# Optimization experiments

Hardware: AMD Instinct MI355X
Metric: run time of the kernel (lower is better)

The kernel has to match this reference:

```python
import jax, jax.numpy as jnp
import numpy as np
import math

N_FFT = 1024
HOP = 256
WIN = 1024
SR = 16000
N_MELS = 80
N_STFT = N_FFT // 2 + 1  # 513
B = 16
T_AUDIO = 320000


def _hz_to_mel_slaney(f):
    f = np.asarray(f, dtype=np.float64)
    mels = 3.0 * f / 200.0
    min_log_hz = 1000.0
    min_log_mel = 15.0
    logstep = math.log(6.4) / 27.0
    return np.where(f >= min_log_hz, min_log_mel + np.log(np.maximum(f, 1e-10) / min_log_hz) / logstep, mels)


def _mel_to_hz_slaney(m):
    m = np.asarray(m, dtype=np.float64)
    freqs = 200.0 * m / 3.0
    min_log_hz = 1000.0
    min_log_mel = 15.0
    logstep = math.log(6.4) / 27.0
    return np.where(m >= min_log_mel, min_log_hz * np.exp(logstep * (m - min_log_mel)), freqs)


def _melscale_fbanks(n_freqs, f_min, f_max, n_mels, sample_rate):
    # torchaudio.functional.melscale_fbanks with norm='slaney', mel_scale='slaney'
    all_freqs = np.linspace(0.0, sample_rate / 2.0, n_freqs)
    m_pts = np.linspace(_hz_to_mel_slaney(f_min), _hz_to_mel_slaney(f_max), n_mels + 2)
    f_pts = _mel_to_hz_slaney(m_pts)
    f_diff = f_pts[1:] - f_pts[:-1]                       # (n_mels+1,)
    slopes = f_pts[None, :] - all_freqs[:, None]          # (n_freqs, n_mels+2)
    down = -slopes[:, :-2] / f_diff[:-1]
    up = slopes[:, 2:] / f_diff[1:]
    fb = np.maximum(0.0, np.minimum(down, up))
    enorm = 2.0 / (f_pts[2:n_mels + 2] - f_pts[:n_mels])  # slaney norm
    fb = fb * enorm[None, :]
    return fb.astype(np.float32)                          # (n_freqs, n_mels)


def setup_inputs() -> dict:
    key = jax.random.key(0)
    wav = jax.random.normal(key, (B, 1, T_AUDIO), dtype=jnp.float32)
    # hann window, periodic
    n = np.arange(WIN, dtype=np.float64)
    window = (0.5 - 0.5 * np.cos(2.0 * np.pi * n / WIN)).astype(np.float32)
    mel_fbanks = _melscale_fbanks(N_STFT, 0.0, SR / 2.0, N_MELS, SR)
    k = np.arange(N_STFT, dtype=np.float64)[:, None]
    nn = np.arange(N_FFT, dtype=np.float64)[None, :]
    angle = -2.0 * np.pi * k * nn / N_FFT
    rfft_real_t = np.cos(angle).T.astype(np.float32)      # (n_fft, n_stft)
    rfft_imag_t = np.sin(angle).T.astype(np.float32)
    return {
        "wav_with_channel": wav,
        "window": jnp.asarray(window),
        "mel_fbanks": jnp.asarray(mel_fbanks),
        "rfft_real_t": jnp.asarray(rfft_real_t),
        "rfft_imag_t": jnp.asarray(rfft_imag_t),
    }


def reference(wav_with_channel, window, mel_fbanks, rfft_real_t, rfft_imag_t):
    wav = wav_with_channel[:, 0, :]                       # (B, T)
    pad = N_FFT // 2
    padded = jnp.pad(wav, ((0, 0), (pad, pad)), mode="reflect")
    padded_len = padded.shape[1]
    num_frames = (padded_len - WIN) // HOP + 1
    idx = jnp.arange(num_frames)[:, None] * HOP + jnp.arange(WIN)[None, :]
    frames = padded[:, idx]
    windowed = frames * window
    real = jnp.matmul(windowed, rfft_real_t)              # (B, F, n_stft)
    imag = jnp.matmul(windowed, rfft_imag_t)
    magnitude = jnp.sqrt(real * real + imag * imag)       # power == 1.0
    mel = jnp.matmul(magnitude, mel_fbanks)               # (B, F, n_mels)
    return jnp.transpose(mel, (0, 2, 1))                  # (B, n_mels, F)
```

## Files before the change

kernel.cpp:

```cpp
#include <hip/hip_runtime.h>
#include <cstddef>

#define HOP 256
#define NSTFT 513
#define N_MELS 80
#define T_AUDIO 320000
#define NUM_FRAMES 1251
#define NBATCH 16
#define TOTAL_FRAMES (NBATCH * NUM_FRAMES)

#define LOGSTEP 0.06875177742094913f
#define MEL_MAX 45.24564047f
#define DF 15.625f

__device__ __forceinline__ int reflect_idx(int j) {
    j = (j < 0) ? -j : j;
    j = (j >= T_AUDIO) ? (2 * T_AUDIO - 2 - j) : j;
    return j;
}

__device__ __forceinline__ int m1_of(int k) {
    const float f = k * DF;
    const float mel = (f < 1000.f) ? (3.0f / 200.0f) * f
                                   : 15.0f + logf(f * 1e-3f) * (1.0f / LOGSTEP);
    return (int)floorf(mel * (81.0f / MEL_MAX));
}

__device__ __forceinline__ int swz(int k) {
    return (k & ~15) | ((k ^ (k >> 4)) & 15);
}

#define DPP_XOR1 0xB1
#define DPP_XOR2 0x4E
#define DPP_XOR8 0x128
template<int CTRL>
__device__ __forceinline__ float dppf(float x) {
    return __int_as_float(__builtin_amdgcn_update_dpp(
        0, __float_as_int(x), CTRL, 0xF, 0xF, true));
}

template<class F>
__device__ __forceinline__ void cstage(float (&zr)[2][16], float (&zi)[2][16],
                                       float sg, float twr_, float twi_, F comm) {
    #pragma unroll
    for (int p = 0; p < 2; ++p) {
        #pragma unroll
        for (int r = 0; r < 16; ++r) {
            const float pr  = comm(zr[p][r]);
            const float pim = comm(zi[p][r]);
            const float qr = fmaf(sg, zr[p][r], pr);
            const float qi = fmaf(sg, zi[p][r], pim);
            zr[p][r] = fmaf(qr, twr_, -(qi * twi_));
            zi[p][r] = fmaf(qr, twi_, qi * twr_);
        }
    }
}

__global__ __launch_bounds__(256) void melspec_sfft6_kernel(
    const float* __restrict__ wav,
    const float* __restrict__ window,
    const float* __restrict__ fb,
    const float* __restrict__ cosT,
    const float* __restrict__ sinT,
    float* __restrict__ out)
{
    __shared__ float2 smag[4][512];
    __shared__ float2 wtab[512];
    __shared__ unsigned short ks[84];

    const int tid = threadIdx.x;
    const int lane = tid & 63;
    const int w = tid >> 6;
    const int g0 = (blockIdx.x * 4 + w) * 4;

    const int BREV4[16] = {0,8,4,12,2,10,6,14,1,9,5,13,3,11,7,15};
    const int SIG[16]   = {0,1,3,2,7,6,5,4,15,14,13,12,11,10,9,8};
    const float W16R[8] = {1.0f, 0.92387953251128674f, 0.70710678118654752f, 0.38268343236508977f,
                           0.0f, -0.38268343236508977f, -0.70710678118654752f, -0.92387953251128674f};
    const float W16I[8] = {0.0f, -0.38268343236508977f, -0.70710678118654752f, -0.92387953251128674f,
                           -1.0f, -0.92387953251128674f, -0.70710678118654752f, -0.38268343236508977f};

    for (int k = tid + 1; k <= 512; k += 256) {
        const int mc = m1_of(k);
        const int mp = m1_of(k - 1);
        if (k <= 511) {
            const float wu = (mc <= 79) ? fb[k * N_MELS + mc] : 0.0f;
            const float wd = (mc >= 1 && mc <= 80) ? fb[k * N_MELS + mc - 1] : 0.0f;
            wtab[swz(k)] = make_float2(wu, wd);
        }
        for (int m = mp + 1; m <= mc; ++m) ks[m] = (unsigned short)k;
        if (k == 1) ks[0] = 1;
    }
    __syncthreads();

    unsigned bf0, ff0, bf3;
    {
        const unsigned g = (unsigned)g0;
        bf0 = g / NUM_FRAMES; ff0 = g - bf0 * NUM_FRAMES;
        bf3 = (unsigned)(g0 + 3) / NUM_FRAMES;
    }

    float win[16];
    #pragma unroll
    for (int r = 0; r < 16; ++r) win[r] = window[r * 64 + lane];

    float zr[2][16], zi[2][16];
    if (bf0 == bf3) {
        const float* wb = wav + (size_t)bf0 * T_AUDIO;
        const int base = (int)ff0 * HOP - 512;
        float ch[28];
        #pragma unroll
        for (int c = 0; c < 28; ++c)
            ch[c] = wb[reflect_idx(base + c * 64 + lane)];
        #pragma unroll
        for (int r = 0; r < 16; ++r) {
            zr[0][r] = ch[r]      * win[r];
            zi[0][r] = ch[r + 4]  * win[r];
            zr[1][r] = ch[r + 8]  * win[r];
            zi[1][r] = ch[r + 12] * win[r];
        }
    } else {
        #pragma unroll
        for (int fi = 0; fi < 4; ++fi) {
            const unsigned g = (unsigned)(g0 + fi);
            const unsigned bb = g / NUM_FRAMES;
            const unsigned ffr = g - bb * NUM_FRAMES;
            const float* wb = wav + (size_t)bb * T_AUDIO;
            const int base = (int)ffr * HOP - 512;
            #pragma unroll
            for (int r = 0; r < 16; ++r) {
                const float v = wb[reflect_idx(base + r * 64 + lane)] * win[r];
                if (fi == 0) zr[0][r] = v;
                else if (fi == 1) zi[0][r] = v;
                else if (fi == 2) zr[1][r] = v;
                else zi[1][r] = v;
            }
        }
    }

    const float* twc = cosT + NSTFT;
    const float* tws = sinT + NSTFT;

    const float w1r = twc[lane];
    const float w1i = tws[lane];
    float wkr[16], wki[16];
    wkr[0] = 1.0f; wki[0] = 0.0f;
    #pragma unroll
    for (int k = 1; k < 16; ++k) {
        wkr[k] = wkr[k-1] * w1r - wki[k-1] * w1i;
        wki[k] = wkr[k-1] * w1i + wki[k-1] * w1r;
    }

    float c64[6], s64[6];
    #pragma unroll
    for (int t = 0; t < 6; ++t) {
        const int half = 32 >> t;
        const bool hi = (lane & half) != 0;
        const int jj = (lane & (half - 1)) << (t + 4);
        c64[t] = hi ? twc[jj] : 1.0f;
        s64[t] = hi ? tws[jj] : 0.0f;
    }

    #define CBFLY(ar, ai, br, bi, wr, wi) { \
        const float _tr = (ar) - (br), _ti = (ai) - (bi); \
        (ar) += (br); (ai) += (bi); \
        (br) = _tr * (wr) - _ti * (wi); \
        (bi) = _tr * (wi) + _ti * (wr); }

    #pragma unroll
    for (int p = 0; p < 2; ++p) {
        #pragma unroll
        for (int q = 0; q < 8; ++q) CBFLY(zr[p][q], zi[p][q], zr[p][q+8], zi[p][q+8], W16R[q], W16I[q]);
        #pragma unroll
        for (int g = 0; g < 16; g += 8)
            #pragma unroll
            for (int q = 0; q < 4; ++q) CBFLY(zr[p][g+q], zi[p][g+q], zr[p][g+q+4], zi[p][g+q+4], W16R[2*q], W16I[2*q]);
        #pragma unroll
        for (int g = 0; g < 16; g += 4)
            #pragma unroll
            for (int q = 0; q < 2; ++q) CBFLY(zr[p][g+q], zi[p][g+q], zr[p][g+q+2], zi[p][g+q+2], W16R[4*q], W16I[4*q]);
        #pragma unroll
        for (int g = 0; g < 16; g += 2) CBFLY(zr[p][g], zi[p][g], zr[p][g+1], zi[p][g+1], 1.0f, 0.0f);
    }

    #pragma unroll
    for (int r = 1; r < 16; ++r) {
        const float c1 = wkr[BREV4[r]];
        const float s1 = wki[BREV4[r]];
        #pragma unroll
        for (int p = 0; p < 2; ++p) {
            const float xr = zr[p][r], xi = zi[p][r];
            zr[p][r] = xr * c1 - xi * s1;
            zi[p][r] = xr * s1 + xi * c1;
        }
    }

    {
        float sg;
        sg = (lane & 32) ? -1.0f : 1.0f;
        cstage(zr, zi, sg, c64[0], s64[0], [](float v) { return __shfl_xor(v, 32); });
        sg = (lane & 16) ? -1.0f : 1.0f;
        cstage(zr, zi, sg, c64[1], s64[1], [](float v) { return __shfl_xor(v, 16); });
        sg = (lane & 8) ? -1.0f : 1.0f;
        cstage(zr, zi, sg, c64[2], s64[2], [](float v) { return dppf<DPP_XOR8>(v); });
        sg = (lane & 4) ? -1.0f : 1.0f;
        cstage(zr, zi, sg, c64[3], s64[3], [](float v) { return __shfl_xor(v, 4); });
        sg = (lane & 2) ? -1.0f : 1.0f;
        cstage(zr, zi, sg, c64[4], s64[4], [](float v) { return dppf<DPP_XOR2>(v); });
        sg = (lane & 1) ? -1.0f : 1.0f;
        cstage(zr, zi, sg, c64[5], s64[5], [](float v) { return dppf<DPP_XOR1>(v); });
    }

    const int k2 = (int)(__brev((unsigned)lane) >> 26);
    const int lp0 = (int)(__brev((unsigned)((64 - k2) & 63)) >> 26);
    #pragma unroll
    for (int p = 0; p < 2; ++p) {
        #pragma unroll
        for (int r = 0; r < 16; ++r) {
            float cx, cy;
            if (r == 0) { cx = __shfl(zr[p][0], lp0); cy = __shfl(zi[p][0], lp0); }
            else        { cx = __shfl_xor(zr[p][SIG[r]], 63); cy = __shfl_xor(zi[p][SIG[r]], 63); }
            const int k1 = BREV4[r];
            const int k = k2 * 16 + k1;
            if (k <= 511) {
                const float a = zr[p][r], b = zi[p][r];
                const float magA = 0.5f * sqrtf((a + cx) * (a + cx) + (b - cy) * (b - cy));
                const float magB = 0.5f * sqrtf((b + cy) * (b + cy) + (a - cx) * (a - cx));
                smag[w][(k & ~15) | (k1 ^ (k2 & 15))] = make_float2(magA, magB);
            }
        }
        #pragma unroll
        for (int i = 0; i < 3; ++i) {
            const int t2 = lane + 64 * i;
            if (t2 < 2 * N_MELS) {
                const int m = 79 - (t2 >> 1);
                const int fi = t2 & 1;
                const int ka = ks[m], kb = ks[m + 1], kc = ks[m + 2];
                float acc = 0.0f;
                for (int k = ka; k < kc; ++k) {
                    const int sl = swz(k);
                    const float2 mg = smag[w][sl];
                    const float2 wt = wtab[sl];
                    acc = fmaf(fi ? mg.y : mg.x, (k < kb) ? wt.x : wt.y, acc);
                }
                const unsigned g = (unsigned)(g0 + 2 * p + fi);
                const unsigned bb = g / NUM_FRAMES;
                const unsigned ff = g - bb * NUM_FRAMES;
                out[((size_t)bb * N_MELS + m) * NUM_FRAMES + ff] = acc;
            }
        }
    }
}

extern "C" void kernel_launch(void* const* d_in, const int* in_sizes, int n_in,
                              void* d_out, int out_size, void* d_ws, size_t ws_size,
                              hipStream_t stream) {
    const float* wav    = (const float*)d_in[0];
    const float* window = (const float*)d_in[1];
    const float* fb     = (const float*)d_in[2];
    const float* cosT   = (const float*)d_in[3];
    const float* sinT   = (const float*)d_in[4];
    float* out = (float*)d_out;

    const int blocks = TOTAL_FRAMES / 16;
    melspec_sfft6_kernel<<<blocks, 256, 0, stream>>>(wav, window, fb, cosT, sinT, out);
}
```

Baseline: 53.58 us.

## Compute mel filterbank via per-wave prefix sums instead of per-mel loops

Replaces the per-mel serial loop over FFT bins, which had variable trip counts and caused divergence, with a prefix-sum formulation. Each lane computes local weighted partial sums over its 16 bins. A wave-level scan across bin groups then produces cumulative sums written to shared memory, and each mel is obtained from three prefix lookups. The change also adds a fast unreflected path for interior frame loads and an occupancy hint in the launch bounds. It trades the divergent loops for extra shuffles and LDS traffic, and the prefix differencing may cost some float precision.

```diff
diff --git a/kernel.cpp b/kernel.cpp
--- a/kernel.cpp
+++ b/kernel.cpp
@@ -30,6 +30,10 @@
     return (k & ~15) | ((k ^ (k >> 4)) & 15);
 }
 
+__device__ __forceinline__ float bperm(int addr, float v) {
+    return __int_as_float(__builtin_amdgcn_ds_bpermute(addr, __float_as_int(v)));
+}
+
 #define DPP_XOR1 0xB1
 #define DPP_XOR2 0x4E
 #define DPP_XOR8 0x128
@@ -56,7 +60,7 @@
     }
 }
 
-__global__ __launch_bounds__(256) void melspec_sfft6_kernel(
+__global__ __launch_bounds__(256, 5) void melspec_ps_kernel(
     const float* __restrict__ wav,
     const float* __restrict__ window,
     const float* __restrict__ fb,
@@ -64,7 +68,7 @@
     const float* __restrict__ sinT,
     float* __restrict__ out)
 {
-    __shared__ float2 smag[4][512];
+    __shared__ float2 psb[4][512];
     __shared__ float2 wtab[512];
     __shared__ unsigned short ks[84];
 
@@ -80,16 +84,19 @@
     const float W16I[8] = {0.0f, -0.38268343236508977f, -0.70710678118654752f, -0.92387953251128674f,
                            -1.0f, -0.92387953251128674f, -0.70710678118654752f, -0.38268343236508977f};
 
-    for (int k = tid + 1; k <= 512; k += 256) {
+    if (tid == 0) { ks[81] = 512; ks[82] = 512; }
+    for (int k = tid; k <= 512; k += 256) {
         const int mc = m1_of(k);
-        const int mp = m1_of(k - 1);
         if (k <= 511) {
-            const float wu = (mc <= 79) ? fb[k * N_MELS + mc] : 0.0f;
-            const float wd = (mc >= 1 && mc <= 80) ? fb[k * N_MELS + mc - 1] : 0.0f;
+            const float wu = (mc >= 0 && mc <= 79) ? 0.5f * fb[k * N_MELS + mc] : 0.0f;
+            const float wd = (mc >= 1 && mc <= 80) ? 0.5f * fb[k * N_MELS + mc - 1] : 0.0f;
             wtab[swz(k)] = make_float2(wu, wd);
         }
-        for (int m = mp + 1; m <= mc; ++m) ks[m] = (unsigned short)k;
-        if (k == 1) ks[0] = 1;
+        if (k >= 1) {
+            const int mp = m1_of(k - 1);
+            for (int m = mp + 1; m <= mc; ++m) ks[m] = (unsigned short)k;
+            if (k == 1) ks[0] = 1;
+        }
     }
     __syncthreads();
 
@@ -109,9 +116,15 @@
         const float* wb = wav + (size_t)bf0 * T_AUDIO;
         const int base = (int)ff0 * HOP - 512;
         float ch[28];
-        #pragma unroll
-        for (int c = 0; c < 28; ++c)
-            ch[c] = wb[reflect_idx(base + c * 64 + lane)];
+        if (base >= 0 && base + 27 * 64 + 63 < T_AUDIO) {
+            #pragma unroll
+            for (int c = 0; c < 28; ++c)
+                ch[c] = wb[base + c * 64 + lane];
+        } else {
+            #pragma unroll
+            for (int c = 0; c < 28; ++c)
+                ch[c] = wb[reflect_idx(base + c * 64 + lane)];
+        }
         #pragma unroll
         for (int r = 0; r < 16; ++r) {
             zr[0][r] = ch[r]      * win[r];
@@ -211,44 +224,72 @@
         cstage(zr, zi, sg, c64[5], s64[5], [](float v) { return dppf<DPP_XOR1>(v); });
     }
 
-    const int k2 = (int)(__brev((unsigned)lane) >> 26);
-    const int lp0 = (int)(__brev((unsigned)((64 - k2) & 63)) >> 26);
+    const int k2c = (int)(__brev((unsigned)lane) >> 26);
+    const int lp0 = (int)(__brev((unsigned)((64 - k2c) & 63)) >> 26);
+    const int k2m16 = (k2c & 31) * 16;
+    const int k2c4 = k2c << 2;
+
     #pragma unroll
     for (int p = 0; p < 2; ++p) {
+        float mgA[16], mgB[16];
         #pragma unroll
         for (int r = 0; r < 16; ++r) {
             float cx, cy;
             if (r == 0) { cx = __shfl(zr[p][0], lp0); cy = __shfl(zi[p][0], lp0); }
             else        { cx = __shfl_xor(zr[p][SIG[r]], 63); cy = __shfl_xor(zi[p][SIG[r]], 63); }
-            const int k1 = BREV4[r];
-            const int k = k2 * 16 + k1;
-            if (k <= 511) {
-                const float a = zr[p][r], b = zi[p][r];
-                const float magA = 0.5f * sqrtf((a + cx) * (a + cx) + (b - cy) * (b - cy));
-                const float magB = 0.5f * sqrtf((b + cy) * (b + cy) + (a - cx) * (a - cx));
-                smag[w][(k & ~15) | (k1 ^ (k2 & 15))] = make_float2(magA, magB);
-            }
-        }
-        #pragma unroll
-        for (int i = 0; i < 3; ++i) {
-            const int t2 = lane + 64 * i;
-            if (t2 < 2 * N_MELS) {
-                const int m = 79 - (t2 >> 1);
-                const int fi = t2 & 1;
-                const int ka = ks[m], kb = ks[m + 1], kc = ks[m + 2];
-                float acc = 0.0f;
-                for (int k = ka; k < kc; ++k) {
-                    const int sl = swz(k);
-                    const float2 mg = smag[w][sl];
-                    const float2 wt = wtab[sl];
-                    acc = fmaf(fi ? mg.y : mg.x, (k < kb) ? wt.x : wt.y, acc);
+            const float a = zr[p][r], b = zi[p][r];
+            mgA[r] = sqrtf((a + cx) * (a + cx) + (b - cy) * (b - cy));
+            mgB[r] = sqrtf((b + cy) * (b + cy) + (a - cx) * (a - cx));
+        }
+
+        auto mel_pass = [&](const float (&mg)[16], int fi) {
+            float ru = 0.f, rd = 0.f;
+            #pragma unroll
+            for (int k1 = 0; k1 < 16; ++k1) {
+                const int r = BREV4[k1];
+                const float2 wt = wtab[swz(k2m16 + k1)];
+                ru = fmaf(mg[r], wt.x, ru);
+                rd = fmaf(mg[r], wt.y, rd);
+            }
+            float vu = bperm(k2c4, ru), vd = bperm(k2c4, rd);
+            const float tu = vu, td = vd;
+            #pragma unroll
+            for (int s = 1; s <= 16; s <<= 1) {
+                const float au = __shfl_up(vu, s);
+                const float ad = __shfl_up(vd, s);
+                if (lane >= s) { vu += au; vd += ad; }
+            }
+            const float eu = bperm(k2c4, vu - tu);
+            const float ed = bperm(k2c4, vd - td);
+            if (!(lane & 1)) {
+                float pu = eu, pd = ed;
+                #pragma unroll
+                for (int k1 = 0; k1 < 16; ++k1) {
+                    const int r = BREV4[k1];
+                    const float2 wt = wtab[swz(k2m16 + k1)];
+                    pu = fmaf(mg[r], wt.x, pu);
+                    pd = fmaf(mg[r], wt.y, pd);
+                    psb[w][swz(k2m16 + k1)] = make_float2(pu, pd);
                 }
-                const unsigned g = (unsigned)(g0 + 2 * p + fi);
-                const unsigned bb = g / NUM_FRAMES;
-                const unsigned ff = g - bb * NUM_FRAMES;
-                out[((size_t)bb * N_MELS + m) * NUM_FRAMES + ff] = acc;
-            }
-        }
+            }
+            #pragma unroll
+            for (int ii = 0; ii < 2; ++ii) {
+                const int m = lane + 64 * ii;
+                if (m < N_MELS) {
+                    const int ka = ks[m], kb = ks[m + 1], kc = ks[m + 2];
+                    const float2 Pa = psb[w][swz(ka - 1)];
+                    const float2 Pb = psb[w][swz(kb - 1)];
+                    const float2 Pc = psb[w][swz(kc - 1)];
+                    const float mel = (Pb.x - Pa.x) + (Pc.y - Pb.y);
+                    const unsigned g = (unsigned)(g0 + 2 * p + fi);
+                    const unsigned bb = g / NUM_FRAMES;
+                    const unsigned ff = g - bb * NUM_FRAMES;
+                    out[((size_t)bb * N_MELS + m) * NUM_FRAMES + ff] = mel;
+                }
+            }
+        };
+        mel_pass(mgA, 0);
+        mel_pass(mgB, 1);
     }
 }
 
@@ -263,5 +304,5 @@
     float* out = (float*)d_out;
 
     const int blocks = TOTAL_FRAMES / 16;
-    melspec_sfft6_kernel<<<blocks, 256, 0, stream>>>(wav, window, fb, cosT, sinT, out);
-}
+    melspec_ps_kernel<<<blocks, 256, 0, stream>>>(wav, window, fb, cosT, sinT, out);
+}
```

After: 133.9 us. 150% more time.

## Premultiply mel weights into LDS products, use permlane swaps and fast-path loads

Applied to the files above, without the earlier changes.

The magnitude stage now multiplies each bin's magnitude by its two filterbank weights (with the 0.5 scale folded into the table) and stores the products in two per-wave LDS arrays. The mel reduction then only sums selected products using two accumulators instead of doing FMAs with separate weight loads. The first two FFT stages use permlane32/16 swap builtins when available instead of ds_bpermute shuffles, and interior frames skip the reflect-index computation. In exchange, LDS use doubles to 36 KB per block, which may reduce occupancy.

```diff
diff --git a/kernel.cpp b/kernel.cpp
--- a/kernel.cpp
+++ b/kernel.cpp
@@ -30,6 +30,23 @@
     return (k & ~15) | ((k ^ (k >> 4)) & 15);
 }
 
+__device__ __forceinline__ float plsum32(float v) {
+#if __has_builtin(__builtin_amdgcn_permlane32_swap)
+    auto r = __builtin_amdgcn_permlane32_swap(__float_as_int(v), __float_as_int(v), false, false);
+    return __int_as_float(r[0]) + __int_as_float(r[1]);
+#else
+    return v + __shfl_xor(v, 32);
+#endif
+}
+__device__ __forceinline__ float plsum16(float v) {
+#if __has_builtin(__builtin_amdgcn_permlane16_swap)
+    auto r = __builtin_amdgcn_permlane16_swap(__float_as_int(v), __float_as_int(v), false, false);
+    return __int_as_float(r[0]) + __int_as_float(r[1]);
+#else
+    return v + __shfl_xor(v, 16);
+#endif
+}
+
 #define DPP_XOR1 0xB1
 #define DPP_XOR2 0x4E
 #define DPP_XOR8 0x128
@@ -56,7 +73,24 @@
     }
 }
 
-__global__ __launch_bounds__(256) void melspec_sfft6_kernel(
+template<class FS>
+__device__ __forceinline__ void cstage_sum(float (&zr)[2][16], float (&zi)[2][16],
+                                           float m2, float twr_, float twi_, FS sumf) {
+    #pragma unroll
+    for (int p = 0; p < 2; ++p) {
+        #pragma unroll
+        for (int r = 0; r < 16; ++r) {
+            const float sR = sumf(zr[p][r]);
+            const float sI = sumf(zi[p][r]);
+            const float qr = fmaf(m2, zr[p][r], sR);
+            const float qi = fmaf(m2, zi[p][r], sI);
+            zr[p][r] = fmaf(qr, twr_, -(qi * twi_));
+            zi[p][r] = fmaf(qr, twi_, qi * twr_);
+        }
+    }
+}
+
+__global__ __launch_bounds__(256) void melspec_prod_kernel(
     const float* __restrict__ wav,
     const float* __restrict__ window,
     const float* __restrict__ fb,
@@ -64,7 +98,8 @@
     const float* __restrict__ sinT,
     float* __restrict__ out)
 {
-    __shared__ float2 smag[4][512];
+    __shared__ float2 prodA[4][512];
+    __shared__ float2 prodB[4][512];
     __shared__ float2 wtab[512];
     __shared__ unsigned short ks[84];
 
@@ -80,16 +115,19 @@
     const float W16I[8] = {0.0f, -0.38268343236508977f, -0.70710678118654752f, -0.92387953251128674f,
                            -1.0f, -0.92387953251128674f, -0.70710678118654752f, -0.38268343236508977f};
 
-    for (int k = tid + 1; k <= 512; k += 256) {
+    if (tid == 0) { ks[81] = 512; ks[82] = 512; }
+    for (int k = tid; k <= 512; k += 256) {
         const int mc = m1_of(k);
-        const int mp = m1_of(k - 1);
         if (k <= 511) {
-            const float wu = (mc <= 79) ? fb[k * N_MELS + mc] : 0.0f;
-            const float wd = (mc >= 1 && mc <= 80) ? fb[k * N_MELS + mc - 1] : 0.0f;
+            const float wu = (mc >= 0 && mc <= 79) ? 0.5f * fb[k * N_MELS + mc] : 0.0f;
+            const float wd = (mc >= 1 && mc <= 80) ? 0.5f * fb[k * N_MELS + mc - 1] : 0.0f;
             wtab[swz(k)] = make_float2(wu, wd);
         }
-        for (int m = mp + 1; m <= mc; ++m) ks[m] = (unsigned short)k;
-        if (k == 1) ks[0] = 1;
+        if (k >= 1) {
+            const int mp = m1_of(k - 1);
+            for (int m = mp + 1; m <= mc; ++m) ks[m] = (unsigned short)k;
+            if (k == 1) ks[0] = 1;
+        }
     }
     __syncthreads();
 
@@ -109,9 +147,15 @@
         const float* wb = wav + (size_t)bf0 * T_AUDIO;
         const int base = (int)ff0 * HOP - 512;
         float ch[28];
-        #pragma unroll
-        for (int c = 0; c < 28; ++c)
-            ch[c] = wb[reflect_idx(base + c * 64 + lane)];
+        if (base >= 0 && base + 27 * 64 + 63 < T_AUDIO) {
+            #pragma unroll
+            for (int c = 0; c < 28; ++c)
+                ch[c] = wb[base + c * 64 + lane];
+        } else {
+            #pragma unroll
+            for (int c = 0; c < 28; ++c)
+                ch[c] = wb[reflect_idx(base + c * 64 + lane)];
+        }
         #pragma unroll
         for (int r = 0; r < 16; ++r) {
             zr[0][r] = ch[r]      * win[r];
@@ -196,11 +240,11 @@
     }
 
     {
+        cstage_sum(zr, zi, (lane & 32) ? -2.0f : 0.0f, c64[0], s64[0],
+                   [](float v) { return plsum32(v); });
+        cstage_sum(zr, zi, (lane & 16) ? -2.0f : 0.0f, c64[1], s64[1],
+                   [](float v) { return plsum16(v); });
         float sg;
-        sg = (lane & 32) ? -1.0f : 1.0f;
-        cstage(zr, zi, sg, c64[0], s64[0], [](float v) { return __shfl_xor(v, 32); });
-        sg = (lane & 16) ? -1.0f : 1.0f;
-        cstage(zr, zi, sg, c64[1], s64[1], [](float v) { return __shfl_xor(v, 16); });
         sg = (lane & 8) ? -1.0f : 1.0f;
         cstage(zr, zi, sg, c64[2], s64[2], [](float v) { return dppf<DPP_XOR8>(v); });
         sg = (lane & 4) ? -1.0f : 1.0f;
@@ -213,6 +257,9 @@
 
     const int k2 = (int)(__brev((unsigned)lane) >> 26);
     const int lp0 = (int)(__brev((unsigned)((64 - k2) & 63)) >> 26);
+    const int k2m16 = (k2 & 31) * 16;
+    const bool hasbin = (k2 < 32);
+
     #pragma unroll
     for (int p = 0; p < 2; ++p) {
         #pragma unroll
@@ -220,33 +267,39 @@
             float cx, cy;
             if (r == 0) { cx = __shfl(zr[p][0], lp0); cy = __shfl(zi[p][0], lp0); }
             else        { cx = __shfl_xor(zr[p][SIG[r]], 63); cy = __shfl_xor(zi[p][SIG[r]], 63); }
-            const int k1 = BREV4[r];
-            const int k = k2 * 16 + k1;
-            if (k <= 511) {
-                const float a = zr[p][r], b = zi[p][r];
-                const float magA = 0.5f * sqrtf((a + cx) * (a + cx) + (b - cy) * (b - cy));
-                const float magB = 0.5f * sqrtf((b + cy) * (b + cy) + (a - cx) * (a - cx));
-                smag[w][(k & ~15) | (k1 ^ (k2 & 15))] = make_float2(magA, magB);
+            const float a = zr[p][r], b = zi[p][r];
+            const float magA = sqrtf((a + cx) * (a + cx) + (b - cy) * (b - cy));
+            const float magB = sqrtf((b + cy) * (b + cy) + (a - cx) * (a - cx));
+            if (hasbin) {
+                const int sl = swz(k2m16 + BREV4[r]);
+                const float2 wt = wtab[sl];
+                prodA[w][sl] = make_float2(magA * wt.x, magA * wt.y);
+                prodB[w][sl] = make_float2(magB * wt.x, magB * wt.y);
             }
         }
-        #pragma unroll
-        for (int i = 0; i < 3; ++i) {
-            const int t2 = lane + 64 * i;
+
+        #pragma unroll
+        for (int ii = 0; ii < 3; ++ii) {
+            const int t2 = lane + 64 * ii;
             if (t2 < 2 * N_MELS) {
                 const int m = 79 - (t2 >> 1);
                 const int fi = t2 & 1;
+                const float2* P = fi ? prodB[w] : prodA[w];
                 const int ka = ks[m], kb = ks[m + 1], kc = ks[m + 2];
-                float acc = 0.0f;
-                for (int k = ka; k < kc; ++k) {
-                    const int sl = swz(k);
-                    const float2 mg = smag[w][sl];
-                    const float2 wt = wtab[sl];
-                    acc = fmaf(fi ? mg.y : mg.x, (k < kb) ? wt.x : wt.y, acc);
+                float acc0 = 0.0f, acc1 = 0.0f;
+                for (int k = ka; k < kc; k += 2) {
+                    const float2 p0 = P[swz(k)];
+                    acc0 += (k < kb) ? p0.x : p0.y;
+                    const int kn = k + 1;
+                    if (kn < kc) {
+                        const float2 p1 = P[swz(kn)];
+                        acc1 += (kn < kb) ? p1.x : p1.y;
+                    }
                 }
                 const unsigned g = (unsigned)(g0 + 2 * p + fi);
                 const unsigned bb = g / NUM_FRAMES;
                 const unsigned ff = g - bb * NUM_FRAMES;
-                out[((size_t)bb * N_MELS + m) * NUM_FRAMES + ff] = acc;
+                out[((size_t)bb * N_MELS + m) * NUM_FRAMES + ff] = acc0 + acc1;
             }
         }
     }
@@ -263,5 +316,5 @@
     float* out = (float*)d_out;
 
     const int blocks = TOTAL_FRAMES / 16;
-    melspec_sfft6_kernel<<<blocks, 256, 0, stream>>>(wav, window, fb, cosT, sinT, out);
-}
+    melspec_prod_kernel<<<blocks, 256, 0, stream>>>(wav, window, fb, cosT, sinT, out);
+}
```

New measurement: 56.44 us. 1.05x slower.

## Replace per-mel loop with load-balanced CSR mel accumulation via LDS atomics

Applied to the files above, without the earlier changes.

Replaces the per-mel variable-length inner loop, where lanes handling wide high-frequency mel bands dominate, with a flat CSR-like entry table of about 1022 nonzero weights. Each lane processes a fixed 16 entries, keeps running sums per mel segment, and flushes them with shared-memory atomicAdd into a per-wave mel buffer. This is meant to remove the divergence and imbalance of the old loop. A second change skips reflect index math when the frame window lies fully inside the audio. In exchange it adds LDS atomics, an extra zeroing pass, and a larger shared table.

```diff
diff --git a/kernel.cpp b/kernel.cpp
--- a/kernel.cpp
+++ b/kernel.cpp
@@ -56,7 +56,7 @@
     }
 }
 
-__global__ __launch_bounds__(256) void melspec_sfft6_kernel(
+__global__ __launch_bounds__(256) void melspec_csr_kernel(
     const float* __restrict__ wav,
     const float* __restrict__ window,
     const float* __restrict__ fb,
@@ -65,7 +65,8 @@
     float* __restrict__ out)
 {
     __shared__ float2 smag[4][512];
-    __shared__ float2 wtab[512];
+    __shared__ float2 ewi[1024];
+    __shared__ float  smel[4][N_MELS][2];
     __shared__ unsigned short ks[84];
 
     const int tid = threadIdx.x;
@@ -80,16 +81,35 @@
     const float W16I[8] = {0.0f, -0.38268343236508977f, -0.70710678118654752f, -0.92387953251128674f,
                            -1.0f, -0.92387953251128674f, -0.70710678118654752f, -0.38268343236508977f};
 
-    for (int k = tid + 1; k <= 512; k += 256) {
-        const int mc = m1_of(k);
-        const int mp = m1_of(k - 1);
-        if (k <= 511) {
-            const float wu = (mc <= 79) ? fb[k * N_MELS + mc] : 0.0f;
-            const float wd = (mc >= 1 && mc <= 80) ? fb[k * N_MELS + mc - 1] : 0.0f;
-            wtab[swz(k)] = make_float2(wu, wd);
-        }
-        for (int m = mp + 1; m <= mc; ++m) ks[m] = (unsigned short)k;
-        if (k == 1) ks[0] = 1;
+    if (tid == 0) { ks[81] = 512; ks[82] = 512; }
+    for (int k = tid; k <= 512; k += 256) {
+        if (k >= 1) {
+            const int mc = m1_of(k);
+            const int mp = m1_of(k - 1);
+            for (int m = mp + 1; m <= mc; ++m) ks[m] = (unsigned short)k;
+            if (k == 1) ks[0] = 1;
+        }
+    }
+    __syncthreads();
+
+    const int E = (int)ks[80] + 508;
+    for (int e = E + tid; e < 1024; e += 256) {
+        const int pos = ((e & 15) << 6) | (e >> 4);
+        ewi[pos] = make_float2(0.0f, __uint_as_float(((unsigned)swz(1) << 7) | 0u));
+    }
+    for (int k = 1 + tid; k <= 511; k += 256) {
+        const int m1 = m1_of(k);
+        const unsigned kid = (unsigned)swz(k) << 7;
+        if (m1 <= 79) {
+            const int e = (int)ks[m1 + 1] + k - 4;
+            const int pos = ((e & 15) << 6) | (e >> 4);
+            ewi[pos] = make_float2(fb[k * N_MELS + m1], __uint_as_float(kid | (unsigned)m1));
+        }
+        if (m1 >= 1 && m1 <= 80) {
+            const int e = (int)ks[m1] + k - 4;
+            const int pos = ((e & 15) << 6) | (e >> 4);
+            ewi[pos] = make_float2(fb[k * N_MELS + m1 - 1], __uint_as_float(kid | (unsigned)(m1 - 1)));
+        }
     }
     __syncthreads();
 
@@ -109,9 +129,15 @@
         const float* wb = wav + (size_t)bf0 * T_AUDIO;
         const int base = (int)ff0 * HOP - 512;
         float ch[28];
-        #pragma unroll
-        for (int c = 0; c < 28; ++c)
-            ch[c] = wb[reflect_idx(base + c * 64 + lane)];
+        if (base >= 0 && base + 27 * 64 + 63 < T_AUDIO) {
+            #pragma unroll
+            for (int c = 0; c < 28; ++c)
+                ch[c] = wb[base + c * 64 + lane];
+        } else {
+            #pragma unroll
+            for (int c = 0; c < 28; ++c)
+                ch[c] = wb[reflect_idx(base + c * 64 + lane)];
+        }
         #pragma unroll
         for (int r = 0; r < 16; ++r) {
             zr[0][r] = ch[r]      * win[r];
@@ -216,6 +242,12 @@
     #pragma unroll
     for (int p = 0; p < 2; ++p) {
         #pragma unroll
+        for (int z = 0; z < 3; ++z) {
+            const int t2 = lane + 64 * z;
+            if (t2 < 2 * N_MELS) ((float*)smel[w])[t2] = 0.0f;
+        }
+
+        #pragma unroll
         for (int r = 0; r < 16; ++r) {
             float cx, cy;
             if (r == 0) { cx = __shfl(zr[p][0], lp0); cy = __shfl(zi[p][0], lp0); }
@@ -229,24 +261,42 @@
                 smag[w][(k & ~15) | (k1 ^ (k2 & 15))] = make_float2(magA, magB);
             }
         }
-        #pragma unroll
-        for (int i = 0; i < 3; ++i) {
-            const int t2 = lane + 64 * i;
+
+        {
+            float accA = 0.0f, accB = 0.0f;
+            int prev_m = -1;
+            #pragma unroll
+            for (int j = 0; j < 16; ++j) {
+                const float2 en = ewi[(j << 6) | lane];
+                const unsigned id = __float_as_uint(en.y);
+                const int m = (int)(id & 127u);
+                const int ksw = (int)(id >> 7);
+                if (m != prev_m) {
+                    if (prev_m >= 0) {
+                        atomicAdd(&smel[w][prev_m][0], accA);
+                        atomicAdd(&smel[w][prev_m][1], accB);
+                    }
+                    accA = 0.0f; accB = 0.0f; prev_m = m;
+                }
+                const float2 mg = smag[w][ksw];
+                accA = fmaf(mg.x, en.x, accA);
+                accB = fmaf(mg.y, en.x, accB);
+            }
+            atomicAdd(&smel[w][prev_m][0], accA);
+            atomicAdd(&smel[w][prev_m][1], accB);
+        }
+
+        #pragma unroll
+        for (int ii = 0; ii < 3; ++ii) {
+            const int t2 = lane + 64 * ii;
             if (t2 < 2 * N_MELS) {
-                const int m = 79 - (t2 >> 1);
+                const int m = t2 >> 1;
                 const int fi = t2 & 1;
-                const int ka = ks[m], kb = ks[m + 1], kc = ks[m + 2];
-                float acc = 0.0f;
-                for (int k = ka; k < kc; ++k) {
-                    const int sl = swz(k);
-                    const float2 mg = smag[w][sl];
-                    const float2 wt = wtab[sl];
-                    acc = fmaf(fi ? mg.y : mg.x, (k < kb) ? wt.x : wt.y, acc);
-                }
+                const float mel = smel[w][m][fi];
                 const unsigned g = (unsigned)(g0 + 2 * p + fi);
                 const unsigned bb = g / NUM_FRAMES;
                 const unsigned ff = g - bb * NUM_FRAMES;
-                out[((size_t)bb * N_MELS + m) * NUM_FRAMES + ff] = acc;
+                out[((size_t)bb * N_MELS + m) * NUM_FRAMES + ff] = mel;
             }
         }
     }
@@ -263,5 +313,5 @@
     float* out = (float*)d_out;
 
     const int blocks = TOTAL_FRAMES / 16;
-    melspec_sfft6_kernel<<<blocks, 256, 0, stream>>>(wav, window, fb, cosT, sinT, out);
-}
+    melspec_csr_kernel<<<blocks, 256, 0, stream>>>(wav, window, fb, cosT, sinT, out);
+}
```

Measured after the change: 64.56 us. 1.2x slower.
